# Optimization experiments

Measured on AMD Instinct MI355X. Metric: run time of the kernel, lower is better.

Reference implementation:

```python
import jax
import jax.numpy as jnp
import numpy as np
from jax import lax

B = 4096        # batch
DATA = 16       # data_dim (control channels)
HID = 64        # hidden_dim
VFW = 128       # vf_hidden_dim
LAB = 10        # label_dim
T = 201         # number of time points in ts (span [0,1])
DT0 = 0.01      # fixed step size -> 100 Heun steps over [0,1]
N_STEPS = 100


def _linear_init(key, out_f, in_f):
    kw, kb = jax.random.split(key)
    lim = 1.0 / np.sqrt(in_f)
    w = jax.random.uniform(kw, (out_f, in_f), minval=-lim, maxval=lim, dtype=jnp.float32)
    b = jax.random.uniform(kb, (out_f,), minval=-lim, maxval=lim, dtype=jnp.float32)
    return w, b


def setup_inputs() -> dict:
    key = jax.random.key(0)
    ks = jax.random.split(key, 8)
    ts = jnp.linspace(0.0, 1.0, T, dtype=jnp.float32)
    coeffs = jax.random.normal(ks[0], (T - 1, DATA, 4), dtype=jnp.float32) * 0.1
    x0 = jax.random.normal(ks[1], (B, DATA), dtype=jnp.float32)
    lin1_w, lin1_b = _linear_init(ks[2], HID, DATA)
    mlp_w0, mlp_b0 = _linear_init(ks[3], VFW, HID)
    mlp_w1, mlp_b1 = _linear_init(ks[4], VFW, VFW)
    mlp_w2, mlp_b2 = _linear_init(ks[5], HID * DATA, VFW)
    lin2_w, lin2_b = _linear_init(ks[6], LAB, HID)
    return dict(ts=ts, coeffs=coeffs, x0=x0,
                lin1_w=lin1_w, lin1_b=lin1_b,
                mlp_w0=mlp_w0, mlp_b0=mlp_b0,
                mlp_w1=mlp_w1, mlp_b1=mlp_b1,
                mlp_w2=mlp_w2, mlp_b2=mlp_b2,
                lin2_w=lin2_w, lin2_b=lin2_b)


def reference(ts, coeffs, x0, lin1_w, lin1_b, mlp_w0, mlp_b0, mlp_w1, mlp_b1,
              mlp_w2, mlp_b2, lin2_w, lin2_b):
    def control_deriv(t):
        # cubic spline segment lookup: coeffs[idx] is (DATA, 4)
        idx = jnp.clip(jnp.searchsorted(ts[1:], t), 0, T - 2)
        dt = t - ts[idx]
        c = coeffs[idx]
        return c[:, 0] + dt * (c[:, 1] + dt * (c[:, 2] + dt * c[:, 3]))  # (DATA,)

    def vector_field(t, y):
        # MLP: HID -> VFW -> VFW -> HID*DATA (relu, relu, tanh)
        h = jax.nn.relu(y @ mlp_w0.T + mlp_b0)
        h = jax.nn.relu(h @ mlp_w1.T + mlp_b1)
        h = jnp.tanh(h @ mlp_w2.T + mlp_b2)
        vf = h.reshape(-1, HID, DATA)            # (B, HID, DATA)
        cd = control_deriv(t)                    # (DATA,)
        return jnp.einsum('bhd,d->bh', vf, cd)   # dy/dt, (B, HID)

    y0 = x0 @ lin1_w.T + lin1_b                  # (B, HID)
    t0 = ts[0]
    t1 = ts[-1]
    dt = (t1 - t0) / N_STEPS                     # == DT0 for [0,1] span

    def step(carry, _):
        y, t = carry
        k1 = vector_field(t, y)
        k2 = vector_field(t + dt, y + dt * k1)
        y_next = y + 0.5 * dt * (k1 + k2)        # Heun (explicit trapezoidal)
        return (y_next, t + dt), None

    (y_final, _), _ = lax.scan(step, (y0, t0), None, length=N_STEPS)
    logits = y_final @ lin2_w.T + lin2_b
    return jax.nn.softmax(logits, axis=-1)       # (B, LAB)
```

## Files before the change

kernel.cpp:

```cpp
#include <hip/hip_runtime.h>

#define BTOT   4096
#define DATA   16
#define HID    64
#define VFW    128
#define LAB    10
#define TPTS   201
#define NSEG   200
#define NSTEPS 100
#define MT     16
#define NBLK   (BTOT / MT)
#define YS     68

typedef __attribute__((ext_vector_type(8))) short short8;
typedef __attribute__((ext_vector_type(4))) float f32x4;
typedef __attribute__((ext_vector_type(2))) unsigned uint2v;

#define LOG2E  1.4426950408889634f
#define K2L    (2.0f * LOG2E)

__device__ __forceinline__ short f2bf(float f) {
    unsigned u = __builtin_bit_cast(unsigned, f);
    u = (u + 0x7FFFu + ((u >> 16) & 1u)) >> 16;
    return (short)u;
}

__device__ __forceinline__ unsigned cvt_pk_bf16(float lo, float hi) {
    unsigned r;
    asm("v_cvt_pk_bf16_f32 %0, %1, %2" : "=v"(r) : "v"(lo), "v"(hi));
    return r;
}

__device__ __forceinline__ float exp2_raw(float x) {
#if __has_builtin(__builtin_amdgcn_exp2f)
    return __builtin_amdgcn_exp2f(x);
#else
    return exp2f(x);
#endif
}

__device__ __forceinline__ int hidx(int row, int kb, int off) {
    return row * 136 + ((kb ^ (row & 3)) << 5) + off;
}
__device__ __forceinline__ int yidx(int row, int kb, int off) {
    return row * 72 + ((kb ^ (row & 1)) << 5) + off;
}

__global__ void pack_w(const float* __restrict__ W, short* __restrict__ outp,
                       int N, int K, float scale) {
    int tid = blockIdx.x * blockDim.x + threadIdx.x;
    int KS = K >> 5;
    int total = (N >> 4) * KS * 64;
    if (tid >= total) return;
    int ln = tid & 63;
    int fs = tid >> 6;
    int ks = fs % KS;
    int nt = fs / KS;
    int n  = nt * 16 + (ln & 15);
    int k0 = ks * 32 + (ln >> 4) * 8;
    const float* src = W + n * K + k0;
    short8 v;
#pragma unroll
    for (int j = 0; j < 8; ++j) v[j] = f2bf(scale * src[j]);
    *(((short8*)outp) + tid) = v;
}

__global__ __launch_bounds__(1024, 4) void cde_main(
    const float* __restrict__ ts_g,  const float* __restrict__ coeffs,
    const float* __restrict__ x0,    const float* __restrict__ lin1_w,
    const float* __restrict__ lin1_b,
    const float* __restrict__ b0g,   const float* __restrict__ b1g,
    const float* __restrict__ b2g,   const float* __restrict__ l2w,
    const float* __restrict__ l2b,
    const short8* __restrict__ w0p,  const short8* __restrict__ w1p,
    const short8* __restrict__ w2p,  float* __restrict__ out)
{
    __shared__ float ts_sh[TPTS];
    __shared__ float ttab[NSTEPS + 1];
    __shared__ float cdtab[(NSTEPS + 1) * DATA];
    __shared__ float cdqtab[(NSTEPS + 1) * 4];
    __shared__ float y32[MT * YS];
    __shared__ __align__(16) short ybf[MT * 72];
    __shared__ __align__(16) short h1bf[MT * 136];
    __shared__ __align__(16) short h2bf[MT * 136];
    __shared__ float b2s[HID * DATA];
    __shared__ __align__(16) short w0f[1024 * 8];
    __shared__ __align__(16) short w1f[2048 * 8];
    __shared__ float lgts[MT * 12];

    const int tid  = threadIdx.x;
    const int lane = tid & 63;
    const int wave = tid >> 6;
    const int lm   = lane & 15;
    const int lg   = lane >> 4;
    const int row0 = blockIdx.x * MT;

    for (int i = tid; i < TPTS; i += 1024) ts_sh[i] = ts_g[i];
    __syncthreads();

    const float dtv = (ts_sh[TPTS - 1] - ts_sh[0]) / 100.0f;
    const float half_dt = 0.5f * dtv;

    if (tid == 0) {
        float tv = ts_sh[0];
        ttab[0] = tv;
        for (int s = 0; s < NSTEPS; ++s) { tv = tv + dtv; ttab[s + 1] = tv; }
    }
    for (int i = tid; i < HID * DATA; i += 1024) b2s[i] = K2L * b2g[i];
    for (int i = tid; i < 1024; i += 1024) ((short8*)w0f)[i] = w0p[i];
    for (int i = tid; i < 2048; i += 1024) ((short8*)w1f)[i] = w1p[i];

    const int ycol = wave * 4 + lg;
    float yreg;
    {
        float s = lin1_b[ycol];
        const float* xr = x0 + (row0 + lm) * DATA;
        const float* wr = lin1_w + ycol * DATA;
#pragma unroll
        for (int k = 0; k < DATA; ++k) s += xr[k] * wr[k];
        yreg = s;
        ybf[yidx(lm, ycol >> 5, ycol & 31)] = f2bf(s);
    }
    __syncthreads();

    for (int idx = tid; idx < (NSTEPS + 1) * DATA; idx += 1024) {
        float tv = ttab[idx >> 4];
        int d = idx & 15;
        int g  = (int)(tv * 200.0f);
        int i0 = g - 2; i0 = i0 < 0 ? 0 : (i0 > 196 ? 196 : i0);
        float v0 = ts_sh[i0 + 1], v1 = ts_sh[i0 + 2], v2 = ts_sh[i0 + 3], v3 = ts_sh[i0 + 4];
        int aidx = i0 + (v0 < tv) + (v1 < tv) + (v2 < tv) + (v3 < tv);
        aidx = aidx > (NSEG - 1) ? (NSEG - 1) : aidx;
        float dtl = tv - ts_sh[aidx];
        const f32x4 cc = *(const f32x4*)(coeffs + (aidx * DATA + d) * 4);
        cdtab[idx] = cc[0] + dtl * (cc[1] + dtl * (cc[2] + dtl * cc[3]));
    }
    __syncthreads();
    for (int idx = tid; idx < (NSTEPS + 1) * 4; idx += 1024) {
        const f32x4 c = *(const f32x4*)&cdtab[idx * 4];
        cdqtab[idx] = (c[0] + c[1]) + (c[2] + c[3]);
    }

    short8 w2r[4][4];
#pragma unroll
    for (int i = 0; i < 4; ++i)
#pragma unroll
        for (int ks = 0; ks < 4; ++ks)
            w2r[i][ks] = w2p[((wave * 4 + i) * 4 + ks) * 64 + lane];
    const f32x4 bias4 = (wave < 8)
        ? *(const f32x4*)&b0g[wave * 16 + 4 * lg]
        : *(const f32x4*)&b1g[(wave - 8) * 16 + 4 * lg];
    __syncthreads();

    auto evalVF = [&](int tidx) -> float {
        if (wave < 8) {
            short8 yb0 = *(const short8*)&ybf[yidx(lm, 0, lg * 8)];
            short8 yb1 = *(const short8*)&ybf[yidx(lm, 1, lg * 8)];
            short8 ws0 = ((const short8*)w0f)[(wave * 2 + 0) * 64 + lane];
            short8 ws1 = ((const short8*)w0f)[(wave * 2 + 1) * 64 + lane];
            f32x4 acc1 = bias4;
            acc1 = __builtin_amdgcn_mfma_f32_16x16x32_bf16(ws0, yb0, acc1, 0, 0, 0);
            acc1 = __builtin_amdgcn_mfma_f32_16x16x32_bf16(ws1, yb1, acc1, 0, 0, 0);
            int col = wave * 16 + 4 * lg;
            unsigned lo = cvt_pk_bf16(fmaxf(acc1[0], 0.f), fmaxf(acc1[1], 0.f));
            unsigned hi = cvt_pk_bf16(fmaxf(acc1[2], 0.f), fmaxf(acc1[3], 0.f));
            uint2v st; st[0] = lo; st[1] = hi;
            *(uint2v*)&h1bf[hidx(lm, col >> 5, col & 31)] = st;
        }
        __syncthreads();
        const f32x4 cdr = *(const f32x4*)&cdtab[tidx * DATA + 4 * lg];
        const float sumcd = cdqtab[tidx * 4 + lg];
        if (wave >= 8) {
            const int nt = wave - 8;
            f32x4 a = bias4;
            f32x4 b = {0.f, 0.f, 0.f, 0.f};
#pragma unroll
            for (int ks = 0; ks < 2; ++ks) {
                short8 h0 = *(const short8*)&h1bf[hidx(lm, 2 * ks + 0, lg * 8)];
                short8 h1 = *(const short8*)&h1bf[hidx(lm, 2 * ks + 1, lg * 8)];
                short8 ws0 = ((const short8*)w1f)[(nt * 4 + 2 * ks) * 64 + lane];
                short8 ws1 = ((const short8*)w1f)[(nt * 4 + 2 * ks + 1) * 64 + lane];
                a = __builtin_amdgcn_mfma_f32_16x16x32_bf16(ws0, h0, a, 0, 0, 0);
                b = __builtin_amdgcn_mfma_f32_16x16x32_bf16(ws1, h1, b, 0, 0, 0);
            }
            f32x4 acc2 = a + b;
            int col = nt * 16 + 4 * lg;
            unsigned lo = cvt_pk_bf16(fmaxf(acc2[0], 0.f), fmaxf(acc2[1], 0.f));
            unsigned hi = cvt_pk_bf16(fmaxf(acc2[2], 0.f), fmaxf(acc2[3], 0.f));
            uint2v st; st[0] = lo; st[1] = hi;
            *(uint2v*)&h2bf[hidx(lm, col >> 5, col & 31)] = st;
        }
        __syncthreads();
        short8 hb[4];
#pragma unroll
        for (int ks = 0; ks < 4; ++ks)
            hb[ks] = *(const short8*)&h2bf[hidx(lm, ks, lg * 8)];
        float p0, p1, p2, p3;
#pragma unroll
        for (int i = 0; i < 4; ++i) {
            int nb = (wave * 4 + i) * 16 + 4 * lg;
            f32x4 acc = *(const f32x4*)&b2s[nb];
#pragma unroll
            for (int ks = 0; ks < 4; ++ks)
                acc = __builtin_amdgcn_mfma_f32_16x16x32_bf16(w2r[i][ks], hb[ks], acc, 0, 0, 0);
            float csum = 0.f;
#pragma unroll
            for (int r = 0; r < 4; ++r) {
                float e  = exp2_raw(acc[r]);
                float rc = __builtin_amdgcn_rcpf(e + 1.0f);
                csum = __builtin_fmaf(cdr[r], rc, csum);
            }
            float sv = __builtin_fmaf(csum, -2.0f, sumcd);
            if (i == 0) p0 = sv; else if (i == 1) p1 = sv;
            else if (i == 2) p2 = sv; else p3 = sv;
        }
        bool g1 = (lg & 1) != 0;
        float a4 = (lg & 2) ? p2 : p0;
        float b4 = (lg & 2) ? p3 : p1;
        float c4 = (lg & 2) ? p0 : p2;
        float d4 = (lg & 2) ? p1 : p3;
        float pg  = g1 ? b4 : a4;
        float pg1 = g1 ? a4 : b4;
        float pg2 = g1 ? d4 : c4;
        float pg3 = g1 ? c4 : d4;
        float s1  = pg  + __shfl_xor(pg1, 16);
        float s1b = pg2 + __shfl_xor(pg3, 16);
        return s1 + __shfl_xor(s1b, 32);
    };

    const int yboff = yidx(lm, ycol >> 5, ycol & 31);
    for (int s = 0; s < NSTEPS; ++s) {
        float K1 = evalVF(s);
        ybf[yboff] = (short)cvt_pk_bf16(__builtin_fmaf(dtv, K1, yreg), 0.f);
        yreg = __builtin_fmaf(half_dt, K1, yreg);
        __syncthreads();
        float K2 = evalVF(s + 1);
        yreg = __builtin_fmaf(half_dt, K2, yreg);
        ybf[yboff] = (short)cvt_pk_bf16(yreg, 0.f);
        __syncthreads();
    }

    y32[lm * YS + ycol] = yreg;
    __syncthreads();
    if (tid < MT * LAB) {
        int m = tid / LAB, j = tid % LAB;
        float s = l2b[j];
        const float* wr = l2w + j * HID;
#pragma unroll
        for (int h = 0; h < HID; ++h) s += y32[m * YS + h] * wr[h];
        lgts[m * 12 + j] = s;
    }
    __syncthreads();
    if (tid < MT) {
        int m = tid;
        float mx = lgts[m * 12];
#pragma unroll
        for (int j = 1; j < LAB; ++j) mx = fmaxf(mx, lgts[m * 12 + j]);
        float e[LAB]; float sum = 0.f;
#pragma unroll
        for (int j = 0; j < LAB; ++j) { e[j] = __expf(lgts[m * 12 + j] - mx); sum += e[j]; }
#pragma unroll
        for (int j = 0; j < LAB; ++j) out[(row0 + m) * LAB + j] = e[j] / sum;
    }
}

extern "C" void kernel_launch(void* const* d_in, const int* in_sizes, int n_in,
                              void* d_out, int out_size, void* d_ws, size_t ws_size,
                              hipStream_t stream) {
    (void)in_sizes; (void)n_in; (void)out_size; (void)ws_size;
    const float* ts     = (const float*)d_in[0];
    const float* coeffs = (const float*)d_in[1];
    const float* x0     = (const float*)d_in[2];
    const float* lin1_w = (const float*)d_in[3];
    const float* lin1_b = (const float*)d_in[4];
    const float* w0     = (const float*)d_in[5];
    const float* b0     = (const float*)d_in[6];
    const float* w1     = (const float*)d_in[7];
    const float* b1     = (const float*)d_in[8];
    const float* w2     = (const float*)d_in[9];
    const float* b2     = (const float*)d_in[10];
    const float* l2w    = (const float*)d_in[11];
    const float* l2b    = (const float*)d_in[12];

    short* w0pack = (short*)d_ws;
    short* w1pack = (short*)((char*)d_ws + 16384);
    short* w2pack = (short*)((char*)d_ws + 49152);

    pack_w<<<dim3(4),  256, 0, stream>>>(w0, w0pack, 128, 64,  1.0f);
    pack_w<<<dim3(8),  256, 0, stream>>>(w1, w1pack, 128, 128, 1.0f);
    pack_w<<<dim3(64), 256, 0, stream>>>(w2, w2pack, 1024, 128, K2L);
    cde_main<<<dim3(NBLK), 1024, 0, stream>>>(ts, coeffs, x0, lin1_w, lin1_b,
        b0, b1, b2, l2w, l2b,
        (const short8*)w0pack, (const short8*)w1pack, (const short8*)w2pack,
        (float*)d_out);
}
```

Measured before the change: 399.3 us.

## Move one W2 tile per wave to LDS and drop XOR swizzle on activations

One of the four W2 fragment groups per wave now lives in shared memory (a new 64 KB buffer) instead of registers. This cuts VGPR pressure in the 1024-thread block, at the cost of extra LDS reads every vector-field evaluation. The XOR-swizzled indexing for the y/h1/h2 activation buffers is also replaced with plain row-major padded indexing, which simplifies address math but may reintroduce bank conflicts. The final-layer tile computation is factored into a helper lambda.

```diff
diff --git a/kernel.cpp b/kernel.cpp
--- a/kernel.cpp
+++ b/kernel.cpp
@@ -37,13 +37,6 @@
 #else
     return exp2f(x);
 #endif
-}
-
-__device__ __forceinline__ int hidx(int row, int kb, int off) {
-    return row * 136 + ((kb ^ (row & 3)) << 5) + off;
-}
-__device__ __forceinline__ int yidx(int row, int kb, int off) {
-    return row * 72 + ((kb ^ (row & 1)) << 5) + off;
 }
 
 __global__ void pack_w(const float* __restrict__ W, short* __restrict__ outp,
@@ -86,6 +79,7 @@
     __shared__ float b2s[HID * DATA];
     __shared__ __align__(16) short w0f[1024 * 8];
     __shared__ __align__(16) short w1f[2048 * 8];
+    __shared__ __align__(16) short w2f3[4096 * 8];
     __shared__ float lgts[MT * 12];
 
     const int tid  = threadIdx.x;
@@ -119,7 +113,7 @@
 #pragma unroll
         for (int k = 0; k < DATA; ++k) s += xr[k] * wr[k];
         yreg = s;
-        ybf[yidx(lm, ycol >> 5, ycol & 31)] = f2bf(s);
+        ybf[lm * 72 + ycol] = f2bf(s);
     }
     __syncthreads();
 
@@ -141,31 +135,51 @@
         cdqtab[idx] = (c[0] + c[1]) + (c[2] + c[3]);
     }
 
-    short8 w2r[4][4];
-#pragma unroll
-    for (int i = 0; i < 4; ++i)
+    short8 w2r[3][4];
+#pragma unroll
+    for (int i = 0; i < 3; ++i)
 #pragma unroll
         for (int ks = 0; ks < 4; ++ks)
             w2r[i][ks] = w2p[((wave * 4 + i) * 4 + ks) * 64 + lane];
+#pragma unroll
+    for (int ks = 0; ks < 4; ++ks)
+        ((short8*)w2f3)[(wave * 4 + ks) * 64 + lane] =
+            w2p[((wave * 4 + 3) * 4 + ks) * 64 + lane];
     const f32x4 bias4 = (wave < 8)
         ? *(const f32x4*)&b0g[wave * 16 + 4 * lg]
         : *(const f32x4*)&b1g[(wave - 8) * 16 + 4 * lg];
     __syncthreads();
 
+    auto g3tile = [&](short8 wa0, short8 wa1, short8 wa2, short8 wa3,
+                      const short8 (&hb)[4], int nb, const f32x4& cdr) -> float {
+        f32x4 acc = *(const f32x4*)&b2s[nb];
+        acc = __builtin_amdgcn_mfma_f32_16x16x32_bf16(wa0, hb[0], acc, 0, 0, 0);
+        acc = __builtin_amdgcn_mfma_f32_16x16x32_bf16(wa1, hb[1], acc, 0, 0, 0);
+        acc = __builtin_amdgcn_mfma_f32_16x16x32_bf16(wa2, hb[2], acc, 0, 0, 0);
+        acc = __builtin_amdgcn_mfma_f32_16x16x32_bf16(wa3, hb[3], acc, 0, 0, 0);
+        float csum = 0.f;
+#pragma unroll
+        for (int r = 0; r < 4; ++r) {
+            float e  = exp2_raw(acc[r]);
+            float rc = __builtin_amdgcn_rcpf(e + 1.0f);
+            csum = __builtin_fmaf(cdr[r], rc, csum);
+        }
+        return csum;
+    };
+
     auto evalVF = [&](int tidx) -> float {
         if (wave < 8) {
-            short8 yb0 = *(const short8*)&ybf[yidx(lm, 0, lg * 8)];
-            short8 yb1 = *(const short8*)&ybf[yidx(lm, 1, lg * 8)];
+            short8 yb0 = *(const short8*)&ybf[lm * 72 + 0  + lg * 8];
+            short8 yb1 = *(const short8*)&ybf[lm * 72 + 32 + lg * 8];
             short8 ws0 = ((const short8*)w0f)[(wave * 2 + 0) * 64 + lane];
             short8 ws1 = ((const short8*)w0f)[(wave * 2 + 1) * 64 + lane];
             f32x4 acc1 = bias4;
             acc1 = __builtin_amdgcn_mfma_f32_16x16x32_bf16(ws0, yb0, acc1, 0, 0, 0);
             acc1 = __builtin_amdgcn_mfma_f32_16x16x32_bf16(ws1, yb1, acc1, 0, 0, 0);
-            int col = wave * 16 + 4 * lg;
             unsigned lo = cvt_pk_bf16(fmaxf(acc1[0], 0.f), fmaxf(acc1[1], 0.f));
             unsigned hi = cvt_pk_bf16(fmaxf(acc1[2], 0.f), fmaxf(acc1[3], 0.f));
             uint2v st; st[0] = lo; st[1] = hi;
-            *(uint2v*)&h1bf[hidx(lm, col >> 5, col & 31)] = st;
+            *(uint2v*)&h1bf[lm * 136 + wave * 16 + 4 * lg] = st;
         }
         __syncthreads();
         const f32x4 cdr = *(const f32x4*)&cdtab[tidx * DATA + 4 * lg];
@@ -176,44 +190,37 @@
             f32x4 b = {0.f, 0.f, 0.f, 0.f};
 #pragma unroll
             for (int ks = 0; ks < 2; ++ks) {
-                short8 h0 = *(const short8*)&h1bf[hidx(lm, 2 * ks + 0, lg * 8)];
-                short8 h1 = *(const short8*)&h1bf[hidx(lm, 2 * ks + 1, lg * 8)];
+                short8 h0 = *(const short8*)&h1bf[lm * 136 + (2 * ks) * 32 + lg * 8];
+                short8 h1 = *(const short8*)&h1bf[lm * 136 + (2 * ks + 1) * 32 + lg * 8];
                 short8 ws0 = ((const short8*)w1f)[(nt * 4 + 2 * ks) * 64 + lane];
                 short8 ws1 = ((const short8*)w1f)[(nt * 4 + 2 * ks + 1) * 64 + lane];
                 a = __builtin_amdgcn_mfma_f32_16x16x32_bf16(ws0, h0, a, 0, 0, 0);
                 b = __builtin_amdgcn_mfma_f32_16x16x32_bf16(ws1, h1, b, 0, 0, 0);
             }
             f32x4 acc2 = a + b;
-            int col = nt * 16 + 4 * lg;
             unsigned lo = cvt_pk_bf16(fmaxf(acc2[0], 0.f), fmaxf(acc2[1], 0.f));
             unsigned hi = cvt_pk_bf16(fmaxf(acc2[2], 0.f), fmaxf(acc2[3], 0.f));
             uint2v st; st[0] = lo; st[1] = hi;
-            *(uint2v*)&h2bf[hidx(lm, col >> 5, col & 31)] = st;
+            *(uint2v*)&h2bf[lm * 136 + nt * 16 + 4 * lg] = st;
         }
         __syncthreads();
         short8 hb[4];
 #pragma unroll
         for (int ks = 0; ks < 4; ++ks)
-            hb[ks] = *(const short8*)&h2bf[hidx(lm, ks, lg * 8)];
-        float p0, p1, p2, p3;
-#pragma unroll
-        for (int i = 0; i < 4; ++i) {
-            int nb = (wave * 4 + i) * 16 + 4 * lg;
-            f32x4 acc = *(const f32x4*)&b2s[nb];
-#pragma unroll
-            for (int ks = 0; ks < 4; ++ks)
-                acc = __builtin_amdgcn_mfma_f32_16x16x32_bf16(w2r[i][ks], hb[ks], acc, 0, 0, 0);
-            float csum = 0.f;
-#pragma unroll
-            for (int r = 0; r < 4; ++r) {
-                float e  = exp2_raw(acc[r]);
-                float rc = __builtin_amdgcn_rcpf(e + 1.0f);
-                csum = __builtin_fmaf(cdr[r], rc, csum);
-            }
-            float sv = __builtin_fmaf(csum, -2.0f, sumcd);
-            if (i == 0) p0 = sv; else if (i == 1) p1 = sv;
-            else if (i == 2) p2 = sv; else p3 = sv;
-        }
+            hb[ks] = *(const short8*)&h2bf[lm * 136 + ks * 32 + lg * 8];
+        short8 w2l0 = ((const short8*)w2f3)[(wave * 4 + 0) * 64 + lane];
+        short8 w2l1 = ((const short8*)w2f3)[(wave * 4 + 1) * 64 + lane];
+        short8 w2l2 = ((const short8*)w2f3)[(wave * 4 + 2) * 64 + lane];
+        short8 w2l3 = ((const short8*)w2f3)[(wave * 4 + 3) * 64 + lane];
+        const int nb0 = (wave * 4) * 16 + 4 * lg;
+        float c0 = g3tile(w2r[0][0], w2r[0][1], w2r[0][2], w2r[0][3], hb, nb0,      cdr);
+        float c1 = g3tile(w2r[1][0], w2r[1][1], w2r[1][2], w2r[1][3], hb, nb0 + 16, cdr);
+        float c2 = g3tile(w2r[2][0], w2r[2][1], w2r[2][2], w2r[2][3], hb, nb0 + 32, cdr);
+        float c3 = g3tile(w2l0, w2l1, w2l2, w2l3,                     hb, nb0 + 48, cdr);
+        float p0 = __builtin_fmaf(c0, -2.0f, sumcd);
+        float p1 = __builtin_fmaf(c1, -2.0f, sumcd);
+        float p2 = __builtin_fmaf(c2, -2.0f, sumcd);
+        float p3 = __builtin_fmaf(c3, -2.0f, sumcd);
         bool g1 = (lg & 1) != 0;
         float a4 = (lg & 2) ? p2 : p0;
         float b4 = (lg & 2) ? p3 : p1;
@@ -228,7 +235,7 @@
         return s1 + __shfl_xor(s1b, 32);
     };
 
-    const int yboff = yidx(lm, ycol >> 5, ycol & 31);
+    const int yboff = lm * 72 + ycol;
     for (int s = 0; s < NSTEPS; ++s) {
         float K1 = evalVF(s);
         ybf[yboff] = (short)cvt_pk_bf16(__builtin_fmaf(dtv, K1, yreg), 0.f);
```

Result: faster. 390.1 us (-2.3%).
